# Performance work log

Measured on AMD Instinct MI355X. Metric: run time of the kernel, lower is better.

## Reference

```python
import jax, jax.numpy as jnp
import numpy as np

H = 12       # num attention heads
D = 64       # head dim
K = 6        # heads activated: max(1, int(H * top_k_percent)), top_k_percent=0.5
EPS = 1e-12  # BERT LayerNorm eps


def setup_inputs() -> dict:
    key = jax.random.key(0)
    ks = jax.random.split(key, 8)
    hid = H * D
    sc = 0.02
    return {
        'hidden_states': jax.random.normal(ks[0], (8, 1024, hid), jnp.float32),
        'Wq': jax.random.normal(ks[1], (hid, hid), jnp.float32) * sc,
        'bq': jnp.zeros((hid,), jnp.float32),
        'Wk': jax.random.normal(ks[2], (hid, hid), jnp.float32) * sc,
        'bk': jnp.zeros((hid,), jnp.float32),
        'Wv': jax.random.normal(ks[3], (hid, hid), jnp.float32) * sc,
        'bv': jnp.zeros((hid,), jnp.float32),
        'Wr': jax.random.normal(ks[4], (hid, H), jnp.float32) * sc,
        'br': jnp.zeros((H,), jnp.float32),
        'Wo': jax.random.normal(ks[5], (hid, hid), jnp.float32) * sc,
        'bo': jnp.zeros((hid,), jnp.float32),
        'ln_g': jnp.ones((hid,), jnp.float32),
        'ln_b': jnp.zeros((hid,), jnp.float32),
    }


def reference(hidden_states, Wq, bq, Wk, bk, Wv, bv, Wr, br, Wo, bo, ln_g, ln_b):
    B, S, hid = hidden_states.shape
    # Router: mean-pooled tokens -> per-head logits -> straight-through top-k mask
    router_in = hidden_states.mean(axis=1)                      # [B, hid]
    logits = router_in @ Wr + br                                # [B, H]
    _, top_idx = jax.lax.top_k(logits, K)                       # [B, K]
    hard = jax.nn.one_hot(top_idx, H, dtype=logits.dtype).sum(axis=1)  # [B, H]
    head_mask = hard + logits - jax.lax.stop_gradient(logits)   # straight-through
    m = head_mask[:, :, None, None]                             # [B, H, 1, 1]

    def proj(W, b):
        return (hidden_states @ W + b).reshape(B, S, H, D).transpose(0, 2, 1, 3)

    q = proj(Wq, bq) * m
    k = proj(Wk, bk) * m
    v = proj(Wv, bv) * m

    scores = jnp.einsum('bhqd,bhkd->bhqk', q, k) / jnp.sqrt(jnp.float32(D))
    probs = jax.nn.softmax(scores, axis=-1)
    ctx = jnp.einsum('bhqk,bhkd->bhqd', probs, v)               # [B, H, S, D]
    ctx = ctx.transpose(0, 2, 1, 3).reshape(B, S, hid)

    # BertSelfOutput: dense -> (dropout=identity in eval) -> residual -> LayerNorm
    x = ctx @ Wo + bo + hidden_states
    mu = x.mean(axis=-1, keepdims=True)
    var = ((x - mu) ** 2).mean(axis=-1, keepdims=True)
    return ((x - mu) / jnp.sqrt(var + EPS)) * ln_g + ln_b
```

## Files before the change

### kernel.cpp

```cpp
#include <hip/hip_runtime.h>

typedef __bf16 bf16;
typedef __bf16 bf16x2_t __attribute__((ext_vector_type(2)));
typedef __bf16 bf16x4_t __attribute__((ext_vector_type(4)));
typedef __bf16 bf16x8 __attribute__((ext_vector_type(8)));
typedef float  f32x4  __attribute__((ext_vector_type(4)));

__device__ __forceinline__ void async16(const void* g, void* l) {
  __builtin_amdgcn_global_load_lds(
      (__attribute__((address_space(1))) void*)(g),
      (__attribute__((address_space(3))) void*)(l), 16, 0, 0);
}

__device__ __forceinline__ f32x4 mfma16(bf16x8 a, bf16x8 b, f32x4 c) {
  return __builtin_amdgcn_mfma_f32_16x16x32_bf16(a, b, c, 0, 0, 0);
}

__global__ __launch_bounds__(256) void cvt_hs_k(const float* __restrict__ src,
                                                bf16* __restrict__ dst, int n) {
  int i = (blockIdx.x * 256 + threadIdx.x) * 4;
  if (i + 3 < n) {
    float4 v = *(const float4*)(src + i);
    dst[i]     = (bf16)v.x;
    dst[i + 1] = (bf16)v.y;
    dst[i + 2] = (bf16)v.z;
    dst[i + 3] = (bf16)v.w;
  } else {
    for (int j = 0; j < 4 && i + j < n; ++j) dst[i + j] = (bf16)src[i + j];
  }
}

__global__ __launch_bounds__(256) void transpose4_k(
    const float* __restrict__ s0, const float* __restrict__ s1,
    const float* __restrict__ s2, const float* __restrict__ s3,
    bf16* __restrict__ d0, bf16* __restrict__ d1,
    bf16* __restrict__ d2, bf16* __restrict__ d3) {
  __shared__ bf16 tile[32][33];
  int z = blockIdx.z;
  const float* in = (z == 0) ? s0 : (z == 1) ? s1 : (z == 2) ? s2 : s3;
  bf16* out       = (z == 0) ? d0 : (z == 1) ? d1 : (z == 2) ? d2 : d3;
  int c0 = blockIdx.x * 32, r0 = blockIdx.y * 32;
  int t = threadIdx.x;
#pragma unroll
  for (int i = 0; i < 4; ++i) {
    int idx = t + i * 256;
    int r = idx >> 5, c = idx & 31;
    tile[r][c] = (bf16)in[(size_t)(r0 + r) * 768 + (c0 + c)];
  }
  __syncthreads();
#pragma unroll
  for (int i = 0; i < 4; ++i) {
    int idx = t + i * 256;
    int r = idx >> 5, c = idx & 31;
    out[(size_t)(c0 + r) * 768 + (r0 + c)] = tile[c][r];
  }
}

__global__ __launch_bounds__(256) void router_partial_k(const float* __restrict__ hs,
                                                        float* __restrict__ partial) {
  int b = blockIdx.x, g = blockIdx.y, t = threadIdx.x;
  if (t >= 192) return;
  const float* p = hs + ((size_t)b * 1024 + g * 64) * 768 + t * 4;
  float4 a = {0.f, 0.f, 0.f, 0.f};
  for (int s = 0; s < 64; ++s) {
    float4 v = *(const float4*)(p + (size_t)s * 768);
    a.x += v.x; a.y += v.y; a.z += v.z; a.w += v.w;
  }
  *(float4*)(partial + ((size_t)b * 16 + g) * 768 + t * 4) = a;
}

__global__ __launch_bounds__(256) void router_final_k(const float* __restrict__ Wr,
                                                      const float* __restrict__ br,
                                                      const float* __restrict__ partial,
                                                      float* __restrict__ mask) {
  int b = blockIdx.x, t = threadIdx.x;
  __shared__ float mean_s[768];
  __shared__ float lg[12];
  for (int c = t; c < 768; c += 256) {
    float a = 0.f;
    for (int g = 0; g < 16; ++g) a += partial[((size_t)b * 16 + g) * 768 + c];
    mean_s[c] = a * (1.0f / 1024.0f);
  }
  __syncthreads();
  if (t < 12) {
    float a = br[t];
    for (int c = 0; c < 768; ++c) a += mean_s[c] * Wr[c * 12 + t];
    lg[t] = a;
  }
  __syncthreads();
  if (t == 0) {
    unsigned chosen = 0;
    for (int j = 0; j < 6; ++j) {
      int bi = -1; float bv = -1e30f;
      for (int h = 0; h < 12; ++h)
        if (!((chosen >> h) & 1) && lg[h] > bv) { bv = lg[h]; bi = h; }
      chosen |= 1u << bi;
    }
    for (int h = 0; h < 12; ++h) mask[b * 12 + h] = ((chosen >> h) & 1) ? 1.f : 0.f;
  }
}

__global__ __launch_bounds__(256, 3) void gemm_qkv_k(
    const bf16* __restrict__ X, const bf16* __restrict__ Wcat,
    const float* __restrict__ bq, const float* __restrict__ bk, const float* __restrict__ bv,
    const float* __restrict__ mask,
    bf16* __restrict__ Qo, bf16* __restrict__ Ko, bf16* __restrict__ Vto) {
  __shared__ __align__(16) bf16 Al[128 * 64];
  __shared__ __align__(16) bf16 Bl[128 * 64];
  int bid = blockIdx.x;
  int xcd = bid & 7, idx = bid >> 3;
  int nt = idx % 18, mt8 = idx / 18;
  int m0 = (mt8 * 8 + xcd) * 128;
  int n0 = nt * 128;
  int z = nt / 6;
  int nb0 = n0 - z * 768;
  int bb = m0 >> 10, hh0 = nb0 >> 6;
  if (mask[bb * 12 + hh0] == 0.f && mask[bb * 12 + hh0 + 1] == 0.f) return;

  const float* bia = (z == 0) ? bq : (z == 1) ? bk : bv;
  int t = threadIdx.x, w = t >> 6, lane = t & 63, lrow = lane & 15, quad = lane >> 4;
  int wm = (w >> 1) * 64, wn = (w & 1) * 64;

  int srow = t >> 3;
  int sch  = (t & 7) ^ (srow & 7);
  const bf16* aptr[4];
  const bf16* bptr[4];
#pragma unroll
  for (int i = 0; i < 4; ++i) {
    aptr[i] = X    + (size_t)(m0 + i * 32 + srow) * 768 + sch * 8;
    bptr[i] = Wcat + (size_t)(n0 + i * 32 + srow) * 768 + sch * 8;
  }

  int ra_base = wm + lrow, rb_base = wn + lrow;
  const bf16* baA[2];
  const bf16* baB[2];
#pragma unroll
  for (int ks = 0; ks < 2; ++ks) {
    baA[ks] = &Al[ra_base * 64 + (((ks * 4 + quad) ^ (ra_base & 7)) * 8)];
    baB[ks] = &Bl[rb_base * 64 + (((ks * 4 + quad) ^ (rb_base & 7)) * 8)];
  }

  f32x4 acc[4][4];
#pragma unroll
  for (int a = 0; a < 4; ++a)
#pragma unroll
    for (int b = 0; b < 4; ++b) acc[a][b] = (f32x4){0.f, 0.f, 0.f, 0.f};

  for (int k0 = 0; k0 < 768; k0 += 64) {
#pragma unroll
    for (int i = 0; i < 4; ++i) {
      async16(aptr[i], &Al[(i * 256 + t) * 8]);
      aptr[i] += 64;
    }
#pragma unroll
    for (int i = 0; i < 4; ++i) {
      async16(bptr[i], &Bl[(i * 256 + t) * 8]);
      bptr[i] += 64;
    }
    __syncthreads();
    bf16x8 af[2][4], bfr[2][4];
#pragma unroll
    for (int ks = 0; ks < 2; ++ks)
#pragma unroll
      for (int i = 0; i < 4; ++i) {
        af[ks][i]  = *(const bf16x8*)(baA[ks] + i * 1024);
        bfr[ks][i] = *(const bf16x8*)(baB[ks] + i * 1024);
      }
#pragma unroll
    for (int ks = 0; ks < 2; ++ks)
#pragma unroll
      for (int mt = 0; mt < 4; ++mt)
#pragma unroll
        for (int nt2 = 0; nt2 < 4; ++nt2)
          acc[mt][nt2] = mfma16(af[ks][mt], bfr[ks][nt2], acc[mt][nt2]);
    __syncthreads();
  }

  float biasv[4];
#pragma unroll
  for (int nt2 = 0; nt2 < 4; ++nt2) biasv[nt2] = bia[nb0 + wn + nt2 * 16 + lrow];

  if (z == 2) {
#pragma unroll
    for (int mt = 0; mt < 4; ++mt)
#pragma unroll
      for (int nt2 = 0; nt2 < 4; ++nt2) {
        int s_base = m0 + wm + mt * 16 + quad * 4;
        int bb2 = s_base >> 10, s = s_base & 1023;
        int nl = nb0 + wn + nt2 * 16 + lrow;
        int h = nl >> 6, d = nl & 63;
        bf16x4_t pk;
#pragma unroll
        for (int r = 0; r < 4; ++r) pk[r] = (bf16)(acc[mt][nt2][r] + biasv[nt2]);
        *(bf16x4_t*)&Vto[(((size_t)bb2 * 12 + h) * 64 + d) * 1024 + s] = pk;
      }
  } else {
    bf16* Out = (z == 0) ? Qo : Ko;
#pragma unroll
    for (int mt = 0; mt < 4; ++mt)
#pragma unroll
      for (int nt2 = 0; nt2 < 4; ++nt2)
#pragma unroll
        for (int r = 0; r < 4; ++r) {
          int m = m0 + wm + mt * 16 + quad * 4 + r;
          int nl = nb0 + wn + nt2 * 16 + lrow;
          int bb2 = m >> 10, s = m & 1023, h = nl >> 6, d = nl & 63;
          Out[(((size_t)bb2 * 12 + h) * 1024 + s) * 64 + d] =
              (bf16)(acc[mt][nt2][r] + biasv[nt2]);
        }
  }
}

__global__ __launch_bounds__(256, 3) void attn_k(
    const bf16* __restrict__ Q, const bf16* __restrict__ K, const bf16* __restrict__ Vt,
    const float* __restrict__ mask, bf16* __restrict__ ctx) {
  int bh = blockIdx.x, qt = blockIdx.y;
  int b = bh / 12, h = bh % 12;
  int t = threadIdx.x, w = t >> 6, lane = t & 63, lrow = lane & 15, quad = lane >> 4;

  if (mask[bh] == 0.f) {
    for (int i = t; i < 4096; i += 256) {
      int r = i >> 5, c = i & 31;
      size_t e = ((size_t)(b * 1024 + qt * 128 + r)) * 768 + h * 64;
      ((unsigned*)ctx)[e / 2 + c] = 0u;
    }
    return;
  }

  __shared__ __align__(16) bf16 K_lds[128 * 64];
  __shared__ __align__(16) bf16 V_lds[64 * 128];
  __shared__ __align__(16) bf16 P_lds[4][16 * 136];

  const bf16* Qh = Q  + (size_t)bh * 65536;
  const bf16* Kh = K  + (size_t)bh * 65536;
  const bf16* Vh = Vt + (size_t)bh * 65536;

  bf16x8 qf[2][2];
#pragma unroll
  for (int mt = 0; mt < 2; ++mt)
#pragma unroll
    for (int ks = 0; ks < 2; ++ks)
      qf[mt][ks] = *(const bf16x8*)&Qh[(size_t)(qt * 128 + w * 32 + mt * 16 + lrow) * 64 + ks * 32 + quad * 8];

  f32x4 o_acc[2][4];
  float m_i[2][4], l_i[2][4];
#pragma unroll
  for (int mt = 0; mt < 2; ++mt) {
#pragma unroll
    for (int dt = 0; dt < 4; ++dt) o_acc[mt][dt] = (f32x4){0.f, 0.f, 0.f, 0.f};
#pragma unroll
    for (int r = 0; r < 4; ++r) { m_i[mt][r] = -INFINITY; l_i[mt][r] = 0.f; }
  }

  for (int kt = 0; kt < 8; ++kt) {
#pragma unroll
    for (int i = 0; i < 4; ++i) {
      int c = i * 256 + t;
      int r = c >> 3, ch = (c & 7) ^ (r & 7);
      async16(Kh + (size_t)kt * 8192 + r * 64 + ch * 8, &K_lds[c * 8]);
    }
#pragma unroll
    for (int i = 0; i < 4; ++i) {
      int c = i * 256 + t;
      int r = c >> 4, ch = (c & 15) ^ (r & 7);
      async16(Vh + (size_t)r * 1024 + kt * 128 + ch * 8, &V_lds[c * 8]);
    }
    __syncthreads();

#pragma unroll
    for (int mt = 0; mt < 2; ++mt) {
      f32x4 s_acc[8];
#pragma unroll
      for (int nt = 0; nt < 8; ++nt) s_acc[nt] = (f32x4){0.f, 0.f, 0.f, 0.f};
#pragma unroll
      for (int nt = 0; nt < 8; ++nt) {
        int rb = nt * 16 + lrow;
#pragma unroll
        for (int ks = 0; ks < 2; ++ks) {
          bf16x8 kf = *(const bf16x8*)&K_lds[rb * 64 + (((ks * 4 + quad) ^ (rb & 7)) * 8)];
          s_acc[nt] = mfma16(qf[mt][ks], kf, s_acc[nt]);
        }
      }
#pragma unroll
      for (int nt = 0; nt < 8; ++nt) s_acc[nt] = s_acc[nt] * 0.125f;

#pragma unroll
      for (int r = 0; r < 4; ++r) {
        float mx = s_acc[0][r];
#pragma unroll
        for (int nt = 1; nt < 8; ++nt) mx = fmaxf(mx, s_acc[nt][r]);
        mx = fmaxf(mx, __shfl_xor(mx, 1));
        mx = fmaxf(mx, __shfl_xor(mx, 2));
        mx = fmaxf(mx, __shfl_xor(mx, 4));
        mx = fmaxf(mx, __shfl_xor(mx, 8));
        float mold = m_i[mt][r];
        float mnew = fmaxf(mold, mx);
        float alpha = __expf(mold - mnew);
        m_i[mt][r] = mnew;
        float rs = 0.f;
#pragma unroll
        for (int nt = 0; nt < 8; ++nt) {
          float pv = __expf(s_acc[nt][r] - mnew);
          rs += pv;
          P_lds[w][(quad * 4 + r) * 136 + nt * 16 + lrow] = (bf16)pv;
        }
        rs += __shfl_xor(rs, 1);
        rs += __shfl_xor(rs, 2);
        rs += __shfl_xor(rs, 4);
        rs += __shfl_xor(rs, 8);
        l_i[mt][r] = l_i[mt][r] * alpha + rs;
#pragma unroll
        for (int dt = 0; dt < 4; ++dt) o_acc[mt][dt][r] *= alpha;
      }

      bf16x8 pf[4];
#pragma unroll
      for (int ks = 0; ks < 4; ++ks)
        pf[ks] = *(const bf16x8*)&P_lds[w][lrow * 136 + ks * 32 + quad * 8];
#pragma unroll
      for (int dt = 0; dt < 4; ++dt) {
        int rv = dt * 16 + lrow;
#pragma unroll
        for (int ks = 0; ks < 4; ++ks) {
          bf16x8 vf = *(const bf16x8*)&V_lds[rv * 128 + (((ks * 4 + quad) ^ (rv & 7)) * 8)];
          o_acc[mt][dt] = mfma16(pf[ks], vf, o_acc[mt][dt]);
        }
      }
    }
    __syncthreads();
  }

#pragma unroll
  for (int mt = 0; mt < 2; ++mt)
#pragma unroll
    for (int r = 0; r < 4; ++r) {
      float inv = 1.0f / l_i[mt][r];
      int s = qt * 128 + w * 32 + mt * 16 + quad * 4 + r;
#pragma unroll
      for (int dt = 0; dt < 4; ++dt) {
        int d = dt * 16 + lrow;
        ctx[((size_t)(b * 1024 + s)) * 768 + h * 64 + d] = (bf16)(o_acc[mt][dt][r] * inv);
      }
    }
}

__global__ __launch_bounds__(256, 3) void gemm_out_k(
    const bf16* __restrict__ Cx, const bf16* __restrict__ Wot,
    const float* __restrict__ bo, const float* __restrict__ res,
    const float* __restrict__ mask,
    float* __restrict__ xo) {
  __shared__ __align__(16) bf16 Al[128 * 64];
  __shared__ __align__(16) bf16 Bl[128 * 64];
  int bid = blockIdx.x;
  int xcd = bid & 7, idx = bid >> 3;
  int nt = idx % 6, mt8 = idx / 6;
  int m0 = (mt8 * 8 + xcd) * 128;
  int n0 = nt * 128;
  int t = threadIdx.x, w = t >> 6, lane = t & 63, lrow = lane & 15, quad = lane >> 4;
  int wm = (w >> 1) * 64, wn = (w & 1) * 64;

  int bb = m0 >> 10;
  unsigned am = 0;
#pragma unroll
  for (int hh = 0; hh < 12; ++hh)
    am |= (mask[bb * 12 + hh] != 0.f) ? (1u << hh) : 0u;

  int srow = t >> 3;
  int sch  = (t & 7) ^ (srow & 7);
  const bf16* aptr[4];
  const bf16* bptr[4];
#pragma unroll
  for (int i = 0; i < 4; ++i) {
    aptr[i] = Cx  + (size_t)(m0 + i * 32 + srow) * 768 + sch * 8;
    bptr[i] = Wot + (size_t)(n0 + i * 32 + srow) * 768 + sch * 8;
  }
  int ra_base = wm + lrow, rb_base = wn + lrow;
  const bf16* baA[2];
  const bf16* baB[2];
#pragma unroll
  for (int ks = 0; ks < 2; ++ks) {
    baA[ks] = &Al[ra_base * 64 + (((ks * 4 + quad) ^ (ra_base & 7)) * 8)];
    baB[ks] = &Bl[rb_base * 64 + (((ks * 4 + quad) ^ (rb_base & 7)) * 8)];
  }

  f32x4 acc[4][4];
#pragma unroll
  for (int a = 0; a < 4; ++a)
#pragma unroll
    for (int b = 0; b < 4; ++b) acc[a][b] = (f32x4){0.f, 0.f, 0.f, 0.f};

  for (int k0 = 0; k0 < 768; k0 += 64) {
    if (am & (1u << (k0 >> 6))) {
#pragma unroll
      for (int i = 0; i < 4; ++i) async16(aptr[i], &Al[(i * 256 + t) * 8]);
#pragma unroll
      for (int i = 0; i < 4; ++i) async16(bptr[i], &Bl[(i * 256 + t) * 8]);
      __syncthreads();
      bf16x8 af[2][4], bfr[2][4];
#pragma unroll
      for (int ks = 0; ks < 2; ++ks)
#pragma unroll
        for (int i = 0; i < 4; ++i) {
          af[ks][i]  = *(const bf16x8*)(baA[ks] + i * 1024);
          bfr[ks][i] = *(const bf16x8*)(baB[ks] + i * 1024);
        }
#pragma unroll
      for (int ks = 0; ks < 2; ++ks)
#pragma unroll
        for (int mt = 0; mt < 4; ++mt)
#pragma unroll
          for (int nt2 = 0; nt2 < 4; ++nt2)
            acc[mt][nt2] = mfma16(af[ks][mt], bfr[ks][nt2], acc[mt][nt2]);
      __syncthreads();
    }
#pragma unroll
    for (int i = 0; i < 4; ++i) { aptr[i] += 64; bptr[i] += 64; }
  }

  float biasv[4];
#pragma unroll
  for (int nt2 = 0; nt2 < 4; ++nt2) biasv[nt2] = bo[n0 + wn + nt2 * 16 + lrow];

#pragma unroll
  for (int mt = 0; mt < 4; ++mt)
#pragma unroll
    for (int nt2 = 0; nt2 < 4; ++nt2)
#pragma unroll
      for (int r = 0; r < 4; ++r) {
        int m = m0 + wm + mt * 16 + quad * 4 + r;
        int n = n0 + wn + nt2 * 16 + lrow;
        xo[(size_t)m * 768 + n] = acc[mt][nt2][r] + biasv[nt2] + res[(size_t)m * 768 + n];
      }
}

__global__ __launch_bounds__(256) void ln_k(const float* __restrict__ x,
                                            const float* __restrict__ g,
                                            const float* __restrict__ be,
                                            float* __restrict__ out) {
  int row = blockIdx.x, t = threadIdx.x;
  const float* xr = x + (size_t)row * 768;
  float v0 = xr[t], v1 = xr[t + 256], v2 = xr[t + 512];
  float s = v0 + v1 + v2;
  float s2 = v0 * v0 + v1 * v1 + v2 * v2;
#pragma unroll
  for (int off = 32; off > 0; off >>= 1) {
    s  += __shfl_down(s, off);
    s2 += __shfl_down(s2, off);
  }
  __shared__ float red[8];
  if ((t & 63) == 0) { red[(t >> 6) * 2] = s; red[(t >> 6) * 2 + 1] = s2; }
  __syncthreads();
  if (t == 0) {
    float a = 0.f, b2 = 0.f;
    for (int i = 0; i < 4; ++i) { a += red[2 * i]; b2 += red[2 * i + 1]; }
    float mu = a * (1.0f / 768.0f);
    float var = b2 * (1.0f / 768.0f) - mu * mu;
    red[0] = mu;
    red[1] = rsqrtf(var + 1e-12f);
  }
  __syncthreads();
  float mu = red[0], rs = red[1];
  out[(size_t)row * 768 + t]       = (v0 - mu) * rs * g[t]       + be[t];
  out[(size_t)row * 768 + t + 256] = (v1 - mu) * rs * g[t + 256] + be[t + 256];
  out[(size_t)row * 768 + t + 512] = (v2 - mu) * rs * g[t + 512] + be[t + 512];
}

extern "C" void kernel_launch(void* const* d_in, const int* in_sizes, int n_in,
                              void* d_out, int out_size, void* d_ws, size_t ws_size,
                              hipStream_t stream) {
  const float* hs  = (const float*)d_in[0];
  const float* Wq  = (const float*)d_in[1];
  const float* bq  = (const float*)d_in[2];
  const float* Wk  = (const float*)d_in[3];
  const float* bk  = (const float*)d_in[4];
  const float* Wv  = (const float*)d_in[5];
  const float* bv  = (const float*)d_in[6];
  const float* Wr  = (const float*)d_in[7];
  const float* br  = (const float*)d_in[8];
  const float* Wo  = (const float*)d_in[9];
  const float* bo  = (const float*)d_in[10];
  const float* lng = (const float*)d_in[11];
  const float* lnb = (const float*)d_in[12];
  float* out = (float*)d_out;
  dim3 blk(256);

  char* p = (char*)d_ws;
  float* maskp   = (float*)p; p += 512;
  float* partial = (float*)p; p += (size_t)8 * 16 * 768 * 4;
  bf16* hsb  = (bf16*)p; p += (size_t)8192 * 768 * 2;
  bf16* Wcat = (bf16*)p; p += (size_t)2304 * 768 * 2;
  bf16* Wot  = (bf16*)p; p += (size_t)768 * 768 * 2;

  cvt_hs_k<<<dim3(6144), blk, 0, stream>>>(hs, hsb, 6291456);
  transpose4_k<<<dim3(24, 24, 4), blk, 0, stream>>>(
      Wq, Wk, Wv, Wo, Wcat, Wcat + 768 * 768, Wcat + 1536 * 768, Wot);
  router_partial_k<<<dim3(8, 16), blk, 0, stream>>>(hs, partial);
  router_final_k<<<dim3(8), blk, 0, stream>>>(Wr, br, partial, maskp);

  size_t used_common = (size_t)(p - (char*)d_ws);
  size_t need_big = used_common + 3 * (size_t)8192 * 768 * 2;

  if (ws_size >= need_big) {
    char* qk_base = p;
    bf16* Qb  = (bf16*)p; p += (size_t)8192 * 768 * 2;
    bf16* Kb  = (bf16*)p; p += (size_t)8192 * 768 * 2;
    bf16* Vtb = (bf16*)p;
    float* Xb = (float*)qk_base;
    bf16* Ctx = (bf16*)d_out;

    gemm_qkv_k<<<dim3(8 * 8 * 18), blk, 0, stream>>>(hsb, Wcat, bq, bk, bv, maskp, Qb, Kb, Vtb);
    attn_k<<<dim3(96, 8), blk, 0, stream>>>(Qb, Kb, Vtb, maskp, Ctx);
    gemm_out_k<<<dim3(8 * 8 * 6), blk, 0, stream>>>(Ctx, Wot, bo, hs, maskp, Xb);
    ln_k<<<dim3(8192), blk, 0, stream>>>(Xb, lng, lnb, out);
  } else {
    bf16* Qb  = (bf16*)p; p += (size_t)1024 * 768 * 2;
    bf16* Kb  = (bf16*)p; p += (size_t)1024 * 768 * 2;
    bf16* Vtb = (bf16*)p; p += (size_t)1024 * 768 * 2;
    bf16* Ctx = (bf16*)p; p += (size_t)1024 * 768 * 2;
    float* Xb = (float*)p; p += (size_t)1024 * 768 * 4;

    for (int b = 0; b < 8; ++b) {
      const bf16* hsb_b = hsb + (size_t)b * 1024 * 768;
      const float* hs_b = hs + (size_t)b * 1024 * 768;
      float* outb = out + (size_t)b * 1024 * 768;
      gemm_qkv_k<<<dim3(8 * 1 * 18), blk, 0, stream>>>(hsb_b, Wcat, bq, bk, bv, maskp + b * 12, Qb, Kb, Vtb);
      attn_k<<<dim3(12, 8), blk, 0, stream>>>(Qb, Kb, Vtb, maskp + b * 12, Ctx);
      gemm_out_k<<<dim3(8 * 1 * 6), blk, 0, stream>>>(Ctx, Wot, bo, hs_b, maskp + b * 12, Xb);
      ln_k<<<dim3(1024), blk, 0, stream>>>(Xb, lng, lnb, outb);
    }
  }
}
```

Before: 255.7 us.

## Fuse bf16 conversion with router reduction; double-buffer attention K/V tiles

Merges the hidden-state fp32-to-bf16 conversion and the router mean partial sums into one kernel, so the input is read once instead of twice. The attention kernel now uses 64-key tiles in double-buffered LDS, issuing the next tile's async loads before computing on the current one and waiting with vmcnt and raw barriers. The smaller tiles mean more online-softmax rescaling steps per query row. The fused kernel launches only 256 blocks, which may limit bandwidth.

```diff
diff --git a/kernel.cpp b/kernel.cpp
--- a/kernel.cpp
+++ b/kernel.cpp
@@ -16,18 +16,22 @@
   return __builtin_amdgcn_mfma_f32_16x16x32_bf16(a, b, c, 0, 0, 0);
 }
 
-__global__ __launch_bounds__(256) void cvt_hs_k(const float* __restrict__ src,
-                                                bf16* __restrict__ dst, int n) {
-  int i = (blockIdx.x * 256 + threadIdx.x) * 4;
-  if (i + 3 < n) {
-    float4 v = *(const float4*)(src + i);
-    dst[i]     = (bf16)v.x;
-    dst[i + 1] = (bf16)v.y;
-    dst[i + 2] = (bf16)v.z;
-    dst[i + 3] = (bf16)v.w;
-  } else {
-    for (int j = 0; j < 4 && i + j < n; ++j) dst[i + j] = (bf16)src[i + j];
-  }
+__global__ __launch_bounds__(256) void cvt_router_k(const float* __restrict__ hs,
+                                                    bf16* __restrict__ hsb,
+                                                    float* __restrict__ partial) {
+  int b = blockIdx.x, g = blockIdx.y, t = threadIdx.x;
+  if (t >= 192) return;
+  const float* p = hs  + ((size_t)b * 1024 + g * 32) * 768 + t * 4;
+  bf16*        q = hsb + ((size_t)b * 1024 + g * 32) * 768 + t * 4;
+  float4 a = {0.f, 0.f, 0.f, 0.f};
+  for (int s = 0; s < 32; ++s) {
+    float4 v = *(const float4*)(p + (size_t)s * 768);
+    a.x += v.x; a.y += v.y; a.z += v.z; a.w += v.w;
+    bf16x4_t o;
+    o[0] = (bf16)v.x; o[1] = (bf16)v.y; o[2] = (bf16)v.z; o[3] = (bf16)v.w;
+    *(bf16x4_t*)(q + (size_t)s * 768) = o;
+  }
+  *(float4*)(partial + ((size_t)b * 32 + g) * 768 + t * 4) = a;
 }
 
 __global__ __launch_bounds__(256) void transpose4_k(
@@ -56,19 +60,6 @@
   }
 }
 
-__global__ __launch_bounds__(256) void router_partial_k(const float* __restrict__ hs,
-                                                        float* __restrict__ partial) {
-  int b = blockIdx.x, g = blockIdx.y, t = threadIdx.x;
-  if (t >= 192) return;
-  const float* p = hs + ((size_t)b * 1024 + g * 64) * 768 + t * 4;
-  float4 a = {0.f, 0.f, 0.f, 0.f};
-  for (int s = 0; s < 64; ++s) {
-    float4 v = *(const float4*)(p + (size_t)s * 768);
-    a.x += v.x; a.y += v.y; a.z += v.z; a.w += v.w;
-  }
-  *(float4*)(partial + ((size_t)b * 16 + g) * 768 + t * 4) = a;
-}
-
 __global__ __launch_bounds__(256) void router_final_k(const float* __restrict__ Wr,
                                                       const float* __restrict__ br,
                                                       const float* __restrict__ partial,
@@ -78,7 +69,7 @@
   __shared__ float lg[12];
   for (int c = t; c < 768; c += 256) {
     float a = 0.f;
-    for (int g = 0; g < 16; ++g) a += partial[((size_t)b * 16 + g) * 768 + c];
+    for (int g = 0; g < 32; ++g) a += partial[((size_t)b * 32 + g) * 768 + c];
     mean_s[c] = a * (1.0f / 1024.0f);
   }
   __syncthreads();
@@ -227,9 +218,9 @@
     return;
   }
 
-  __shared__ __align__(16) bf16 K_lds[128 * 64];
-  __shared__ __align__(16) bf16 V_lds[64 * 128];
-  __shared__ __align__(16) bf16 P_lds[4][16 * 136];
+  __shared__ __align__(16) bf16 K_lds[2][64 * 64];
+  __shared__ __align__(16) bf16 V_lds[2][64 * 64];
+  __shared__ __align__(16) bf16 P_lds[4][16 * 72];
 
   const bf16* Qh = Q  + (size_t)bh * 65536;
   const bf16* Kh = K  + (size_t)bh * 65536;
@@ -252,43 +243,57 @@
     for (int r = 0; r < 4; ++r) { m_i[mt][r] = -INFINITY; l_i[mt][r] = 0.f; }
   }
 
-  for (int kt = 0; kt < 8; ++kt) {
-#pragma unroll
-    for (int i = 0; i < 4; ++i) {
+  auto STAGE = [&](int bsel, int kt) {
+#pragma unroll
+    for (int i = 0; i < 2; ++i) {
       int c = i * 256 + t;
       int r = c >> 3, ch = (c & 7) ^ (r & 7);
-      async16(Kh + (size_t)kt * 8192 + r * 64 + ch * 8, &K_lds[c * 8]);
-    }
-#pragma unroll
-    for (int i = 0; i < 4; ++i) {
+      async16(Kh + (size_t)(kt * 64 + r) * 64 + ch * 8, &K_lds[bsel][c * 8]);
+    }
+#pragma unroll
+    for (int i = 0; i < 2; ++i) {
       int c = i * 256 + t;
-      int r = c >> 4, ch = (c & 15) ^ (r & 7);
-      async16(Vh + (size_t)r * 1024 + kt * 128 + ch * 8, &V_lds[c * 8]);
-    }
-    __syncthreads();
-
+      int r = c >> 3, ch = (c & 7) ^ (r & 7);
+      async16(Vh + (size_t)r * 1024 + kt * 64 + ch * 8, &V_lds[bsel][c * 8]);
+    }
+  };
+
+  STAGE(0, 0);
+  for (int kt = 0; kt < 16; ++kt) {
+    int cur = kt & 1;
+    if (kt < 15) {
+      STAGE(cur ^ 1, kt + 1);
+      asm volatile("s_waitcnt vmcnt(4)" ::: "memory");
+    } else {
+      asm volatile("s_waitcnt vmcnt(0)" ::: "memory");
+    }
+    __builtin_amdgcn_s_barrier();
+    __builtin_amdgcn_sched_barrier(0);
+
+    const bf16* Kc = &K_lds[cur][0];
+    const bf16* Vc = &V_lds[cur][0];
 #pragma unroll
     for (int mt = 0; mt < 2; ++mt) {
-      f32x4 s_acc[8];
-#pragma unroll
-      for (int nt = 0; nt < 8; ++nt) s_acc[nt] = (f32x4){0.f, 0.f, 0.f, 0.f};
-#pragma unroll
-      for (int nt = 0; nt < 8; ++nt) {
+      f32x4 s_acc[4];
+#pragma unroll
+      for (int nt = 0; nt < 4; ++nt) s_acc[nt] = (f32x4){0.f, 0.f, 0.f, 0.f};
+#pragma unroll
+      for (int nt = 0; nt < 4; ++nt) {
         int rb = nt * 16 + lrow;
 #pragma unroll
         for (int ks = 0; ks < 2; ++ks) {
-          bf16x8 kf = *(const bf16x8*)&K_lds[rb * 64 + (((ks * 4 + quad) ^ (rb & 7)) * 8)];
+          bf16x8 kf = *(const bf16x8*)&Kc[rb * 64 + (((ks * 4 + quad) ^ (rb & 7)) * 8)];
           s_acc[nt] = mfma16(qf[mt][ks], kf, s_acc[nt]);
         }
       }
 #pragma unroll
-      for (int nt = 0; nt < 8; ++nt) s_acc[nt] = s_acc[nt] * 0.125f;
+      for (int nt = 0; nt < 4; ++nt) s_acc[nt] = s_acc[nt] * 0.125f;
 
 #pragma unroll
       for (int r = 0; r < 4; ++r) {
         float mx = s_acc[0][r];
 #pragma unroll
-        for (int nt = 1; nt < 8; ++nt) mx = fmaxf(mx, s_acc[nt][r]);
+        for (int nt = 1; nt < 4; ++nt) mx = fmaxf(mx, s_acc[nt][r]);
         mx = fmaxf(mx, __shfl_xor(mx, 1));
         mx = fmaxf(mx, __shfl_xor(mx, 2));
         mx = fmaxf(mx, __shfl_xor(mx, 4));
@@ -299,10 +304,10 @@
         m_i[mt][r] = mnew;
         float rs = 0.f;
 #pragma unroll
-        for (int nt = 0; nt < 8; ++nt) {
+        for (int nt = 0; nt < 4; ++nt) {
           float pv = __expf(s_acc[nt][r] - mnew);
           rs += pv;
-          P_lds[w][(quad * 4 + r) * 136 + nt * 16 + lrow] = (bf16)pv;
+          P_lds[w][(quad * 4 + r) * 72 + nt * 16 + lrow] = (bf16)pv;
         }
         rs += __shfl_xor(rs, 1);
         rs += __shfl_xor(rs, 2);
@@ -313,21 +318,23 @@
         for (int dt = 0; dt < 4; ++dt) o_acc[mt][dt][r] *= alpha;
       }
 
-      bf16x8 pf[4];
-#pragma unroll
-      for (int ks = 0; ks < 4; ++ks)
-        pf[ks] = *(const bf16x8*)&P_lds[w][lrow * 136 + ks * 32 + quad * 8];
+      bf16x8 pf[2];
+#pragma unroll
+      for (int ks = 0; ks < 2; ++ks)
+        pf[ks] = *(const bf16x8*)&P_lds[w][lrow * 72 + ks * 32 + quad * 8];
 #pragma unroll
       for (int dt = 0; dt < 4; ++dt) {
         int rv = dt * 16 + lrow;
 #pragma unroll
-        for (int ks = 0; ks < 4; ++ks) {
-          bf16x8 vf = *(const bf16x8*)&V_lds[rv * 128 + (((ks * 4 + quad) ^ (rv & 7)) * 8)];
+        for (int ks = 0; ks < 2; ++ks) {
+          bf16x8 vf = *(const bf16x8*)&Vc[rv * 64 + (((ks * 4 + quad) ^ (rv & 7)) * 8)];
           o_acc[mt][dt] = mfma16(pf[ks], vf, o_acc[mt][dt]);
         }
       }
     }
-    __syncthreads();
+    __builtin_amdgcn_sched_barrier(0);
+    __builtin_amdgcn_s_barrier();
+    __builtin_amdgcn_sched_barrier(0);
   }
 
 #pragma unroll
@@ -486,15 +493,14 @@
 
   char* p = (char*)d_ws;
   float* maskp   = (float*)p; p += 512;
-  float* partial = (float*)p; p += (size_t)8 * 16 * 768 * 4;
+  float* partial = (float*)p; p += (size_t)8 * 32 * 768 * 4;
   bf16* hsb  = (bf16*)p; p += (size_t)8192 * 768 * 2;
   bf16* Wcat = (bf16*)p; p += (size_t)2304 * 768 * 2;
   bf16* Wot  = (bf16*)p; p += (size_t)768 * 768 * 2;
 
-  cvt_hs_k<<<dim3(6144), blk, 0, stream>>>(hs, hsb, 6291456);
+  cvt_router_k<<<dim3(8, 32), blk, 0, stream>>>(hs, hsb, partial);
   transpose4_k<<<dim3(24, 24, 4), blk, 0, stream>>>(
       Wq, Wk, Wv, Wo, Wcat, Wcat + 768 * 768, Wcat + 1536 * 768, Wot);
-  router_partial_k<<<dim3(8, 16), blk, 0, stream>>>(hs, partial);
   router_final_k<<<dim3(8), blk, 0, stream>>>(Wr, br, partial, maskp);
 
   size_t used_common = (size_t)(p - (char*)d_ws);
```

New measurement: 276.1 us. 1.08x slower.

## Compact active heads into an index list and launch QKV/attention only for them

Applied to the files above, without the earlier changes.

The router now also writes a compact list of the six active heads per batch. The QKV GEMM and attention kernels are launched over that list instead of masking the full head grid. The QKV GEMM is retiled to 128x64 so each block covers exactly one head; before, a 128-wide tile spanning two heads was computed whenever either head was active. The bf16 conversion of hidden states is fused with the router's partial mean sum, and the router logits are computed with a block-wide shuffle reduction. Attention no longer zero-fills context for inactive heads, so correctness depends on the output GEMM ignoring those columns.

```diff
diff --git a/kernel.cpp b/kernel.cpp
--- a/kernel.cpp
+++ b/kernel.cpp
@@ -16,18 +16,21 @@
   return __builtin_amdgcn_mfma_f32_16x16x32_bf16(a, b, c, 0, 0, 0);
 }
 
-__global__ __launch_bounds__(256) void cvt_hs_k(const float* __restrict__ src,
-                                                bf16* __restrict__ dst, int n) {
-  int i = (blockIdx.x * 256 + threadIdx.x) * 4;
-  if (i + 3 < n) {
-    float4 v = *(const float4*)(src + i);
-    dst[i]     = (bf16)v.x;
-    dst[i + 1] = (bf16)v.y;
-    dst[i + 2] = (bf16)v.z;
-    dst[i + 3] = (bf16)v.w;
-  } else {
-    for (int j = 0; j < 4 && i + j < n; ++j) dst[i + j] = (bf16)src[i + j];
-  }
+__global__ __launch_bounds__(192) void cvt_router_k(const float* __restrict__ hs,
+                                                    bf16* __restrict__ hsb,
+                                                    float* __restrict__ partial) {
+  int b = blockIdx.x, g = blockIdx.y, t = threadIdx.x;
+  const float* p = hs  + ((size_t)b * 1024 + g * 32) * 768 + t * 4;
+  bf16*        q = hsb + ((size_t)b * 1024 + g * 32) * 768 + t * 4;
+  float4 a = {0.f, 0.f, 0.f, 0.f};
+  for (int s = 0; s < 32; ++s) {
+    float4 v = *(const float4*)(p + (size_t)s * 768);
+    a.x += v.x; a.y += v.y; a.z += v.z; a.w += v.w;
+    bf16x4_t o;
+    o[0] = (bf16)v.x; o[1] = (bf16)v.y; o[2] = (bf16)v.z; o[3] = (bf16)v.w;
+    *(bf16x4_t*)(q + (size_t)s * 768) = o;
+  }
+  *(float4*)(partial + ((size_t)b * 32 + g) * 768 + t * 4) = a;
 }
 
 __global__ __launch_bounds__(256) void transpose4_k(
@@ -56,39 +59,45 @@
   }
 }
 
-__global__ __launch_bounds__(256) void router_partial_k(const float* __restrict__ hs,
-                                                        float* __restrict__ partial) {
-  int b = blockIdx.x, g = blockIdx.y, t = threadIdx.x;
-  if (t >= 192) return;
-  const float* p = hs + ((size_t)b * 1024 + g * 64) * 768 + t * 4;
-  float4 a = {0.f, 0.f, 0.f, 0.f};
-  for (int s = 0; s < 64; ++s) {
-    float4 v = *(const float4*)(p + (size_t)s * 768);
-    a.x += v.x; a.y += v.y; a.z += v.z; a.w += v.w;
-  }
-  *(float4*)(partial + ((size_t)b * 16 + g) * 768 + t * 4) = a;
-}
-
 __global__ __launch_bounds__(256) void router_final_k(const float* __restrict__ Wr,
                                                       const float* __restrict__ br,
                                                       const float* __restrict__ partial,
-                                                      float* __restrict__ mask) {
+                                                      float* __restrict__ mask,
+                                                      int* __restrict__ actH) {
   int b = blockIdx.x, t = threadIdx.x;
+  int w = t >> 6;
   __shared__ float mean_s[768];
+  __shared__ float red[4][12];
   __shared__ float lg[12];
   for (int c = t; c < 768; c += 256) {
     float a = 0.f;
-    for (int g = 0; g < 16; ++g) a += partial[((size_t)b * 16 + g) * 768 + c];
+    for (int g = 0; g < 32; ++g) a += partial[((size_t)b * 32 + g) * 768 + c];
     mean_s[c] = a * (1.0f / 1024.0f);
   }
   __syncthreads();
-  if (t < 12) {
-    float a = br[t];
-    for (int c = 0; c < 768; ++c) a += mean_s[c] * Wr[c * 12 + t];
-    lg[t] = a;
-  }
+  float a[12];
+#pragma unroll
+  for (int h = 0; h < 12; ++h) a[h] = 0.f;
+#pragma unroll
+  for (int j = 0; j < 3; ++j) {
+    int c = t + j * 256;
+    float m = mean_s[c];
+    const float* wr = Wr + c * 12;
+#pragma unroll
+    for (int h = 0; h < 12; ++h) a[h] += m * wr[h];
+  }
+#pragma unroll
+  for (int off = 1; off < 64; off <<= 1)
+#pragma unroll
+    for (int h = 0; h < 12; ++h) a[h] += __shfl_xor(a[h], off);
+  if ((t & 63) == 0)
+#pragma unroll
+    for (int h = 0; h < 12; ++h) red[w][h] = a[h];
   __syncthreads();
   if (t == 0) {
+#pragma unroll
+    for (int h = 0; h < 12; ++h)
+      lg[h] = br[h] + red[0][h] + red[1][h] + red[2][h] + red[3][h];
     unsigned chosen = 0;
     for (int j = 0; j < 6; ++j) {
       int bi = -1; float bv = -1e30f;
@@ -96,40 +105,43 @@
         if (!((chosen >> h) & 1) && lg[h] > bv) { bv = lg[h]; bi = h; }
       chosen |= 1u << bi;
     }
-    for (int h = 0; h < 12; ++h) mask[b * 12 + h] = ((chosen >> h) & 1) ? 1.f : 0.f;
+    int k = 0;
+    for (int h = 0; h < 12; ++h) {
+      mask[b * 12 + h] = ((chosen >> h) & 1) ? 1.f : 0.f;
+      if ((chosen >> h) & 1) actH[b * 6 + (k++)] = h;
+    }
   }
 }
 
 __global__ __launch_bounds__(256, 3) void gemm_qkv_k(
     const bf16* __restrict__ X, const bf16* __restrict__ Wcat,
     const float* __restrict__ bq, const float* __restrict__ bk, const float* __restrict__ bv,
-    const float* __restrict__ mask,
+    const int* __restrict__ actH,
     bf16* __restrict__ Qo, bf16* __restrict__ Ko, bf16* __restrict__ Vto) {
   __shared__ __align__(16) bf16 Al[128 * 64];
-  __shared__ __align__(16) bf16 Bl[128 * 64];
-  int bid = blockIdx.x;
-  int xcd = bid & 7, idx = bid >> 3;
-  int nt = idx % 18, mt8 = idx / 18;
-  int m0 = (mt8 * 8 + xcd) * 128;
-  int n0 = nt * 128;
-  int z = nt / 6;
-  int nb0 = n0 - z * 768;
-  int bb = m0 >> 10, hh0 = nb0 >> 6;
-  if (mask[bb * 12 + hh0] == 0.f && mask[bb * 12 + hh0 + 1] == 0.f) return;
+  __shared__ __align__(16) bf16 Bl[64 * 64];
+  int mt64 = blockIdx.x;
+  int slot = blockIdx.y;
+  int z    = blockIdx.z;
+  int b    = mt64 >> 3;
+  int h    = actH[b * 6 + slot];
+  int m0   = mt64 * 128;
+  int nw0  = z * 768 + h * 64;
 
   const float* bia = (z == 0) ? bq : (z == 1) ? bk : bv;
   int t = threadIdx.x, w = t >> 6, lane = t & 63, lrow = lane & 15, quad = lane >> 4;
-  int wm = (w >> 1) * 64, wn = (w & 1) * 64;
+  int wm = (w >> 1) * 64, wn = (w & 1) * 32;
 
   int srow = t >> 3;
   int sch  = (t & 7) ^ (srow & 7);
   const bf16* aptr[4];
-  const bf16* bptr[4];
-#pragma unroll
-  for (int i = 0; i < 4; ++i) {
-    aptr[i] = X    + (size_t)(m0 + i * 32 + srow) * 768 + sch * 8;
-    bptr[i] = Wcat + (size_t)(n0 + i * 32 + srow) * 768 + sch * 8;
-  }
+  const bf16* bptr[2];
+#pragma unroll
+  for (int i = 0; i < 4; ++i)
+    aptr[i] = X + (size_t)(m0 + i * 32 + srow) * 768 + sch * 8;
+#pragma unroll
+  for (int i = 0; i < 2; ++i)
+    bptr[i] = Wcat + (size_t)(nw0 + i * 32 + srow) * 768 + sch * 8;
 
   int ra_base = wm + lrow, rb_base = wn + lrow;
   const bf16* baA[2];
@@ -140,11 +152,11 @@
     baB[ks] = &Bl[rb_base * 64 + (((ks * 4 + quad) ^ (rb_base & 7)) * 8)];
   }
 
-  f32x4 acc[4][4];
+  f32x4 acc[4][2];
 #pragma unroll
   for (int a = 0; a < 4; ++a)
 #pragma unroll
-    for (int b = 0; b < 4; ++b) acc[a][b] = (f32x4){0.f, 0.f, 0.f, 0.f};
+    for (int c = 0; c < 2; ++c) acc[a][c] = (f32x4){0.f, 0.f, 0.f, 0.f};
 
   for (int k0 = 0; k0 < 768; k0 += 64) {
 #pragma unroll
@@ -153,59 +165,56 @@
       aptr[i] += 64;
     }
 #pragma unroll
-    for (int i = 0; i < 4; ++i) {
+    for (int i = 0; i < 2; ++i) {
       async16(bptr[i], &Bl[(i * 256 + t) * 8]);
       bptr[i] += 64;
     }
     __syncthreads();
-    bf16x8 af[2][4], bfr[2][4];
+    bf16x8 af[2][4], bfr[2][2];
+#pragma unroll
+    for (int ks = 0; ks < 2; ++ks) {
+#pragma unroll
+      for (int i = 0; i < 4; ++i) af[ks][i] = *(const bf16x8*)(baA[ks] + i * 1024);
+#pragma unroll
+      for (int j = 0; j < 2; ++j) bfr[ks][j] = *(const bf16x8*)(baB[ks] + j * 1024);
+    }
 #pragma unroll
     for (int ks = 0; ks < 2; ++ks)
 #pragma unroll
-      for (int i = 0; i < 4; ++i) {
-        af[ks][i]  = *(const bf16x8*)(baA[ks] + i * 1024);
-        bfr[ks][i] = *(const bf16x8*)(baB[ks] + i * 1024);
-      }
-#pragma unroll
-    for (int ks = 0; ks < 2; ++ks)
-#pragma unroll
       for (int mt = 0; mt < 4; ++mt)
 #pragma unroll
-        for (int nt2 = 0; nt2 < 4; ++nt2)
+        for (int nt2 = 0; nt2 < 2; ++nt2)
           acc[mt][nt2] = mfma16(af[ks][mt], bfr[ks][nt2], acc[mt][nt2]);
     __syncthreads();
   }
 
-  float biasv[4];
-#pragma unroll
-  for (int nt2 = 0; nt2 < 4; ++nt2) biasv[nt2] = bia[nb0 + wn + nt2 * 16 + lrow];
+  float biasv[2];
+#pragma unroll
+  for (int nt2 = 0; nt2 < 2; ++nt2) biasv[nt2] = bia[h * 64 + wn + nt2 * 16 + lrow];
 
   if (z == 2) {
 #pragma unroll
     for (int mt = 0; mt < 4; ++mt)
 #pragma unroll
-      for (int nt2 = 0; nt2 < 4; ++nt2) {
-        int s_base = m0 + wm + mt * 16 + quad * 4;
-        int bb2 = s_base >> 10, s = s_base & 1023;
-        int nl = nb0 + wn + nt2 * 16 + lrow;
-        int h = nl >> 6, d = nl & 63;
+      for (int nt2 = 0; nt2 < 2; ++nt2) {
+        int s = (m0 + wm + mt * 16 + quad * 4) & 1023;
+        int d = wn + nt2 * 16 + lrow;
         bf16x4_t pk;
 #pragma unroll
         for (int r = 0; r < 4; ++r) pk[r] = (bf16)(acc[mt][nt2][r] + biasv[nt2]);
-        *(bf16x4_t*)&Vto[(((size_t)bb2 * 12 + h) * 64 + d) * 1024 + s] = pk;
+        *(bf16x4_t*)&Vto[(((size_t)b * 12 + h) * 64 + d) * 1024 + s] = pk;
       }
   } else {
     bf16* Out = (z == 0) ? Qo : Ko;
 #pragma unroll
     for (int mt = 0; mt < 4; ++mt)
 #pragma unroll
-      for (int nt2 = 0; nt2 < 4; ++nt2)
+      for (int nt2 = 0; nt2 < 2; ++nt2)
 #pragma unroll
         for (int r = 0; r < 4; ++r) {
-          int m = m0 + wm + mt * 16 + quad * 4 + r;
-          int nl = nb0 + wn + nt2 * 16 + lrow;
-          int bb2 = m >> 10, s = m & 1023, h = nl >> 6, d = nl & 63;
-          Out[(((size_t)bb2 * 12 + h) * 1024 + s) * 64 + d] =
+          int s = (m0 + wm + mt * 16 + quad * 4 + r) & 1023;
+          int d = wn + nt2 * 16 + lrow;
+          Out[(((size_t)b * 12 + h) * 1024 + s) * 64 + d] =
               (bf16)(acc[mt][nt2][r] + biasv[nt2]);
         }
   }
@@ -213,19 +222,12 @@
 
 __global__ __launch_bounds__(256, 3) void attn_k(
     const bf16* __restrict__ Q, const bf16* __restrict__ K, const bf16* __restrict__ Vt,
-    const float* __restrict__ mask, bf16* __restrict__ ctx) {
-  int bh = blockIdx.x, qt = blockIdx.y;
-  int b = bh / 12, h = bh % 12;
+    const int* __restrict__ actH, bf16* __restrict__ ctx) {
+  int ai = blockIdx.x, qt = blockIdx.y;
+  int bb = ai / 6, slot = ai - bb * 6;
+  int h = actH[bb * 6 + slot];
+  int bh = bb * 12 + h;
   int t = threadIdx.x, w = t >> 6, lane = t & 63, lrow = lane & 15, quad = lane >> 4;
-
-  if (mask[bh] == 0.f) {
-    for (int i = t; i < 4096; i += 256) {
-      int r = i >> 5, c = i & 31;
-      size_t e = ((size_t)(b * 1024 + qt * 128 + r)) * 768 + h * 64;
-      ((unsigned*)ctx)[e / 2 + c] = 0u;
-    }
-    return;
-  }
 
   __shared__ __align__(16) bf16 K_lds[128 * 64];
   __shared__ __align__(16) bf16 V_lds[64 * 128];
@@ -339,7 +341,7 @@
 #pragma unroll
       for (int dt = 0; dt < 4; ++dt) {
         int d = dt * 16 + lrow;
-        ctx[((size_t)(b * 1024 + s)) * 768 + h * 64 + d] = (bf16)(o_acc[mt][dt][r] * inv);
+        ctx[((size_t)(bb * 1024 + s)) * 768 + h * 64 + d] = (bf16)(o_acc[mt][dt][r] * inv);
       }
     }
 }
@@ -485,17 +487,17 @@
   dim3 blk(256);
 
   char* p = (char*)d_ws;
-  float* maskp   = (float*)p; p += 512;
-  float* partial = (float*)p; p += (size_t)8 * 16 * 768 * 4;
+  float* maskp = (float*)p; p += 512;
+  int*   actI  = (int*)p;   p += 256;
+  float* partial = (float*)p; p += (size_t)8 * 32 * 768 * 4;
   bf16* hsb  = (bf16*)p; p += (size_t)8192 * 768 * 2;
   bf16* Wcat = (bf16*)p; p += (size_t)2304 * 768 * 2;
   bf16* Wot  = (bf16*)p; p += (size_t)768 * 768 * 2;
 
-  cvt_hs_k<<<dim3(6144), blk, 0, stream>>>(hs, hsb, 6291456);
+  cvt_router_k<<<dim3(8, 32), dim3(192), 0, stream>>>(hs, hsb, partial);
   transpose4_k<<<dim3(24, 24, 4), blk, 0, stream>>>(
       Wq, Wk, Wv, Wo, Wcat, Wcat + 768 * 768, Wcat + 1536 * 768, Wot);
-  router_partial_k<<<dim3(8, 16), blk, 0, stream>>>(hs, partial);
-  router_final_k<<<dim3(8), blk, 0, stream>>>(Wr, br, partial, maskp);
+  router_final_k<<<dim3(8), blk, 0, stream>>>(Wr, br, partial, maskp, actI);
 
   size_t used_common = (size_t)(p - (char*)d_ws);
   size_t need_big = used_common + 3 * (size_t)8192 * 768 * 2;
@@ -508,8 +510,8 @@
     float* Xb = (float*)qk_base;
     bf16* Ctx = (bf16*)d_out;
 
-    gemm_qkv_k<<<dim3(8 * 8 * 18), blk, 0, stream>>>(hsb, Wcat, bq, bk, bv, maskp, Qb, Kb, Vtb);
-    attn_k<<<dim3(96, 8), blk, 0, stream>>>(Qb, Kb, Vtb, maskp, Ctx);
+    gemm_qkv_k<<<dim3(64, 6, 3), blk, 0, stream>>>(hsb, Wcat, bq, bk, bv, actI, Qb, Kb, Vtb);
+    attn_k<<<dim3(48, 8), blk, 0, stream>>>(Qb, Kb, Vtb, actI, Ctx);
     gemm_out_k<<<dim3(8 * 8 * 6), blk, 0, stream>>>(Ctx, Wot, bo, hs, maskp, Xb);
     ln_k<<<dim3(8192), blk, 0, stream>>>(Xb, lng, lnb, out);
   } else {
@@ -523,8 +525,8 @@
       const bf16* hsb_b = hsb + (size_t)b * 1024 * 768;
       const float* hs_b = hs + (size_t)b * 1024 * 768;
       float* outb = out + (size_t)b * 1024 * 768;
-      gemm_qkv_k<<<dim3(8 * 1 * 18), blk, 0, stream>>>(hsb_b, Wcat, bq, bk, bv, maskp + b * 12, Qb, Kb, Vtb);
-      attn_k<<<dim3(12, 8), blk, 0, stream>>>(Qb, Kb, Vtb, maskp + b * 12, Ctx);
+      gemm_qkv_k<<<dim3(8, 6, 3), blk, 0, stream>>>(hsb_b, Wcat, bq, bk, bv, actI + b * 6, Qb, Kb, Vtb);
+      attn_k<<<dim3(6, 8), blk, 0, stream>>>(Qb, Kb, Vtb, actI + b * 6, Ctx);
       gemm_out_k<<<dim3(8 * 1 * 6), blk, 0, stream>>>(Ctx, Wot, bo, hs_b, maskp + b * 12, Xb);
       ln_k<<<dim3(1024), blk, 0, stream>>>(Xb, lng, lnb, outb);
     }
```

Measured after the change: 215.3 us. -15.8%, faster.
